# Kernel optimization log

Measured on AMD Instinct MI355X. Metric: run time of the kernel, lower is better.

## Reference

```python
import jax, jax.numpy as jnp
import numpy as np

N_HEADS = 16

def setup_inputs() -> dict:
    key = jax.random.key(0)
    k1, k2, k3, k4, k5 = jax.random.split(key, 5)
    B, S, D = 2, 2048, 1024
    x = jax.random.normal(k1, (B, S, D), dtype=jnp.float32)
    # parameters scaled ~ fan-in to keep softmax logits sane
    w_in = jax.random.normal(k2, (D, 3 * D), dtype=jnp.float32) * (1.0 / np.sqrt(D))
    b_in = jax.random.normal(k3, (3 * D,), dtype=jnp.float32) * 0.02
    w_out = jax.random.normal(k4, (D, D), dtype=jnp.float32) * (1.0 / np.sqrt(D))
    b_out = jax.random.normal(k5, (D,), dtype=jnp.float32) * 0.02
    return {"x": x, "w_in": w_in, "b_in": b_in, "w_out": w_out, "b_out": b_out,
            "causal_mask": 1}


def reference(x, w_in, b_in, w_out, b_out, causal_mask):
    B, S, D = x.shape
    H = N_HEADS
    dh = D // H
    qkv = x @ w_in + b_in                        # [B, S, 3D]
    q, k, v = jnp.split(qkv, 3, axis=-1)          # each [B, S, D]
    q = q.reshape(B, S, H, dh)
    k = k.reshape(B, S, H, dh)
    v = v.reshape(B, S, H, dh)
    # scores: [B, H, Sq, Sk]
    scores = jnp.einsum("bqhd,bkhd->bhqk", q, k)
    if causal_mask:
        mask = jnp.triu(jnp.ones((S, S), dtype=bool), k=1)
        scores = jnp.where(mask, -jnp.inf, scores)
    scores = scores / jnp.sqrt(jnp.asarray(dh, dtype=scores.dtype))
    weight = jax.nn.softmax(scores, axis=-1)
    out = jnp.einsum("bhqk,bkhd->bqhd", weight, v).reshape(B, S, D)
    return out @ w_out + b_out
```

## Files before the change

kernel.cpp:

```cpp
#include <hip/hip_runtime.h>
#include <hip/hip_bf16.h>

typedef __attribute__((ext_vector_type(8))) short short8;
typedef __attribute__((ext_vector_type(4))) short s16x4;
typedef __attribute__((ext_vector_type(4))) float f32x4;
typedef unsigned short u16;

__device__ inline u16 f2bf(float f) {
    union { float f; unsigned u; } x{f};
    unsigned r = (x.u + 0x7fff + ((x.u >> 16) & 1)) >> 16;
    return (u16)r;
}

__device__ inline unsigned pkbf(float hi, float lo) {
    unsigned a = __builtin_bit_cast(unsigned, hi) + 0x8000u;
    unsigned b = __builtin_bit_cast(unsigned, lo) + 0x8000u;
    return __builtin_amdgcn_perm(a, b, 0x07060302u);
}

__device__ inline void glds16(const u16* g, u16* l) {
    __builtin_amdgcn_global_load_lds(
        (const __attribute__((address_space(1))) void*)g,
        (__attribute__((address_space(3))) void*)l, 16, 0, 0);
}

__global__ __launch_bounds__(256) void prep(const float* __restrict__ x,
                                            const float* __restrict__ w_in,
                                            const float* __restrict__ w_out,
                                            u16* __restrict__ Xb,
                                            u16* __restrict__ WtIn,
                                            u16* __restrict__ WtOut) {
    __shared__ float tile[32][33];
    int bx = blockIdx.x, tid = threadIdx.x;
    if (bx < 4096) {
        int i = (bx * 256 + tid) * 4;
        float4 v = *(const float4*)&x[i];
        uint2 o;
        o.x = (unsigned)f2bf(v.x) | ((unsigned)f2bf(v.y) << 16);
        o.y = (unsigned)f2bf(v.z) | ((unsigned)f2bf(v.w) << 16);
        *(uint2*)&Xb[i] = o;
        return;
    }
    const float* W; u16* Wt; int K, N, n0, k0;
    if (bx < 7168) {
        int b2 = bx - 4096;
        W = w_in; Wt = WtIn; K = 1024; N = 3072;
        n0 = (b2 % 96) * 32; k0 = (b2 / 96) * 32;
    } else {
        int b3 = bx - 7168;
        W = w_out; Wt = WtOut; K = 1024; N = 1024;
        n0 = (b3 & 31) * 32; k0 = (b3 >> 5) * 32;
    }
    int tx = tid & 31, ty = tid >> 5;
    for (int i = 0; i < 32; i += 8)
        tile[ty + i][tx] = W[(size_t)(k0 + ty + i) * N + n0 + tx];
    __syncthreads();
    for (int i = 0; i < 32; i += 8)
        Wt[(size_t)(n0 + ty + i) * K + k0 + tx] = f2bf(tile[tx][ty + i]);
}

__global__ __launch_bounds__(256) void transpose_v(const u16* __restrict__ qkv,
                                                   u16* __restrict__ VT) {
    __shared__ u16 t[32][33];
    int s0 = blockIdx.x * 32, d0 = blockIdx.y * 32, bh = blockIdx.z;
    int b = bh >> 4, h = bh & 15;
    int tx = threadIdx.x, ty = threadIdx.y;
    const u16* Vp = qkv + (size_t)(b * 2048) * 3072 + 2048 + h * 64;
    for (int i = 0; i < 32; i += 8)
        t[ty + i][tx] = Vp[(size_t)(s0 + ty + i) * 3072 + d0 + tx];
    __syncthreads();
    u16* Vr = VT + (size_t)bh * 64 * 2048;
    for (int i = 0; i < 32; i += 8)
        Vr[(size_t)(d0 + ty + i) * 2048 + s0 + tx] = t[tx][ty + i];
}

#define BM 128
#define BN 128
#define BK 64
__global__ __launch_bounds__(256) void gemm_bt(const u16* __restrict__ A,
                                               const u16* __restrict__ Bt,
                                               const float* __restrict__ bias,
                                               void* __restrict__ C,
                                               int M, int N, int K, int c_is_f32,
                                               int qcols, float qscale) {
    __shared__ u16 smem[2 * BM * BK + 2048];
    u16* As = smem;
    u16* Bs = smem + BM * BK;

    int tid = threadIdx.x;
    int wave = tid >> 6, lane = tid & 63;
    int quad = lane >> 4, l16 = lane & 15;
    int wm = (wave >> 1) * 64, wn = (wave & 1) * 64;

    int nm = M / BM, nn = N / BN;
    const int GM = 8;
    int per_group = GM * nn;
    int group = blockIdx.x / per_group;
    int rem = blockIdx.x % per_group;
    int first_m = group * GM;
    int gsz = (nm - first_m < GM) ? (nm - first_m) : GM;
    int m0 = (first_m + rem % gsz) * BM;
    int n0 = (rem / gsz) * BN;

    f32x4 acc[4][4] = {};

    for (int k0 = 0; k0 < K; k0 += BK) {
        __syncthreads();
        for (int i = 0; i < 4; i++) {
            int c = tid + i * 256;
            int r = c >> 3, cc = c & 7;
            int gsrc = (cc ^ (r & 7)) * 8;
            glds16(&A[(size_t)(m0 + r) * K + k0 + gsrc], As + c * 8);
            glds16(&Bt[(size_t)(n0 + r) * K + k0 + gsrc], Bs + c * 8);
        }
        __syncthreads();
        for (int ks = 0; ks < 2; ks++) {
            short8 af[4], bf[4];
            for (int i = 0; i < 4; i++) {
                int row = wm + i * 16 + l16;
                int slot = (ks * 4 + quad) ^ (row & 7);
                af[i] = *(short8*)&As[row * BK + slot * 8];
            }
            for (int j = 0; j < 4; j++) {
                int row = wn + j * 16 + l16;
                int slot = (ks * 4 + quad) ^ (row & 7);
                bf[j] = *(short8*)&Bs[row * BK + slot * 8];
            }
            for (int i = 0; i < 4; i++)
                for (int j = 0; j < 4; j++)
                    acc[i][j] = __builtin_amdgcn_mfma_f32_16x16x32_bf16(
                        af[i], bf[j], acc[i][j], 0, 0, 0);
        }
    }

    if (c_is_f32) {
        for (int i = 0; i < 4; i++)
            for (int j = 0; j < 4; j++) {
                int col = n0 + wn + j * 16 + l16;
                float bv = bias ? bias[col] : 0.f;
                for (int r = 0; r < 4; r++) {
                    int row = m0 + wm + i * 16 + quad * 4 + r;
                    ((float*)C)[(size_t)row * N + col] = acc[i][j][r] + bv;
                }
            }
    } else {
        __syncthreads();
        u16 (*buf)[136] = (u16(*)[136])smem;
        for (int i = 0; i < 4; i++)
            for (int j = 0; j < 4; j++) {
                int col = wn + j * 16 + l16;
                float bv = bias ? bias[n0 + col] : 0.f;
                float scl = (n0 + col < qcols) ? qscale : 1.f;
                for (int r = 0; r < 4; r++)
                    buf[wm + i * 16 + quad * 4 + r][col] =
                        f2bf((acc[i][j][r] + bv) * scl);
            }
        __syncthreads();
        u16* Cb = (u16*)C;
        for (int it = 0; it < 8; it++) {
            int c = tid + it * 256;
            int row = c >> 4, k8 = c & 15;
            uint4 v = *(uint4*)&buf[row][k8 * 8];
            *(uint4*)&Cb[(size_t)(m0 + row) * N + n0 + k8 * 8] = v;
        }
    }
}

__global__ __launch_bounds__(512, 2) void attn_kernel(const u16* __restrict__ qkv,
                                                      const u16* __restrict__ VT,
                                                      u16* __restrict__ out) {
    const int S = 2048, D = 1024, stride = 3072;
    int idx = blockIdx.x;
    int p = idx >> 5, bh = idx & 31;
    int qtb[2] = {15 - p, p};
    int b = bh >> 4, h = bh & 15;
    int tid = threadIdx.x;
    int wave = tid >> 6, lane = tid & 63;
    int quad = lane >> 4, l16 = lane & 15;

    __shared__ u16 Klds[2][2][64 * 64];
    __shared__ u16 Vlds[2][2][64 * 64];
    __shared__ u16 Obuf[8][16][72];

    const u16* Qp = qkv + (size_t)(b * S) * stride + h * 64;
    const u16* Kp = Qp + D;
    const u16* Vtp = VT + (size_t)bh * 64 * S;

    short8 qf[2][2];
    for (int ph = 0; ph < 2; ph++) {
        int qrow = qtb[ph] * 128 + wave * 16 + l16;
        qf[ph][0] = *(const short8*)&Qp[(size_t)qrow * stride + quad * 8];
        qf[ph][1] = *(const short8*)&Qp[(size_t)qrow * stride + 32 + quad * 8];
    }

    int np0 = qtb[0] + 1;
    int ntp = np0 + qtb[1] + 1;

    auto stage = [&](int kt, int bsel, int ch) {
        int c = tid;
        int r = c >> 3, cc = c & 7;
        int gsrc = (cc ^ (r & 7)) * 8;
        glds16(&Kp[(size_t)(kt * 64 + r) * stride + gsrc], &Klds[bsel][ch][c * 8]);
        glds16(&Vtp[(size_t)r * S + kt * 64 + gsrc], &Vlds[bsel][ch][c * 8]);
    };

    stage(0, 0, 0);
    stage(1, 0, 1);

    f32x4 Oa[4] = {}, Ob[4] = {};
    float lsa = 0.f, lsb = 0.f;

    for (int jp = 0; jp < ntp; jp++) {
        int ph = (jp >= np0) ? 1 : 0;
        int j = ph ? jp - np0 : jp;
        int qt = qtb[ph];
        int ka = 2 * j, kb = 2 * j + 1;
        int cur = jp & 1;
        __syncthreads();
        if (jp + 1 < ntp) {
            int jp2 = jp + 1;
            int j2 = (jp2 >= np0) ? jp2 - np0 : jp2;
            stage(2 * j2, cur ^ 1, 0);
            stage(2 * j2 + 1, cur ^ 1, 1);
        }

        short8 kfa[4][2], kfb[4][2];
        for (int nb = 0; nb < 4; nb++) {
            int r = nb * 16 + l16;
            int s0 = ((0 + quad) ^ (r & 7)) * 8;
            int s1 = ((4 + quad) ^ (r & 7)) * 8;
            kfa[nb][0] = *(short8*)&Klds[cur][0][r * 64 + s0];
            kfa[nb][1] = *(short8*)&Klds[cur][0][r * 64 + s1];
            kfb[nb][0] = *(short8*)&Klds[cur][1][r * 64 + s0];
            kfb[nb][1] = *(short8*)&Klds[cur][1][r * 64 + s1];
        }
        f32x4 sta[4], stb[4];
        for (int nb = 0; nb < 4; nb++) {
            f32x4 t = {};
            t = __builtin_amdgcn_mfma_f32_16x16x32_bf16(kfa[nb][0], qf[ph][0], t, 0, 0, 0);
            t = __builtin_amdgcn_mfma_f32_16x16x32_bf16(kfa[nb][1], qf[ph][1], t, 0, 0, 0);
            sta[nb] = t;
            f32x4 u = {};
            u = __builtin_amdgcn_mfma_f32_16x16x32_bf16(kfb[nb][0], qf[ph][0], u, 0, 0, 0);
            u = __builtin_amdgcn_mfma_f32_16x16x32_bf16(kfb[nb][1], qf[ph][1], u, 0, 0, 0);
            stb[nb] = u;
        }

        if (j == qt) {
            int qabs = qt * 128 + wave * 16 + l16;
            for (int nb = 0; nb < 4; nb++) {
                int kba = ka * 64 + nb * 16 + quad * 4;
                int kbb = kb * 64 + nb * 16 + quad * 4;
                for (int r = 0; r < 4; r++) {
                    float ea = __builtin_amdgcn_exp2f(sta[nb][r]);
                    sta[nb][r] = (kba + r <= qabs) ? ea : 0.f;
                    float eb = __builtin_amdgcn_exp2f(stb[nb][r]);
                    stb[nb][r] = (kbb + r <= qabs) ? eb : 0.f;
                }
            }
        } else {
            for (int nb = 0; nb < 4; nb++)
                for (int r = 0; r < 4; r++) {
                    sta[nb][r] = __builtin_amdgcn_exp2f(sta[nb][r]);
                    stb[nb][r] = __builtin_amdgcn_exp2f(stb[nb][r]);
                }
        }

        s16x4 pfa[4], pfb[4];
        for (int nb = 0; nb < 4; nb++) {
            lsa += (sta[nb][0] + sta[nb][1]) + (sta[nb][2] + sta[nb][3]);
            lsb += (stb[nb][0] + stb[nb][1]) + (stb[nb][2] + stb[nb][3]);
            uint2 pk;
            pk.x = pkbf(sta[nb][1], sta[nb][0]);
            pk.y = pkbf(sta[nb][3], sta[nb][2]);
            pfa[nb] = __builtin_bit_cast(s16x4, pk);
            pk.x = pkbf(stb[nb][1], stb[nb][0]);
            pk.y = pkbf(stb[nb][3], stb[nb][2]);
            pfb[nb] = __builtin_bit_cast(s16x4, pk);
        }

        for (int db = 0; db < 4; db++) {
            int rr = db * 16 + l16;
            for (int kc = 0; kc < 4; kc++) {
                int g = kc * 2 + (quad >> 1);
                int slot = g ^ (rr & 7);
                int off = rr * 64 + slot * 8 + (quad & 1) * 4;
                s16x4 vfa = *(s16x4*)&Vlds[cur][0][off];
                Oa[db] = __builtin_amdgcn_mfma_f32_16x16x16bf16_1k(
                    pfa[kc], vfa, Oa[db], 0, 0, 0);
                s16x4 vfb = *(s16x4*)&Vlds[cur][1][off];
                Ob[db] = __builtin_amdgcn_mfma_f32_16x16x16bf16_1k(
                    pfb[kc], vfb, Ob[db], 0, 0, 0);
            }
        }

        if (jp == np0 - 1 || jp == ntp - 1) {
            float v = lsa + lsb;
            v += __shfl_xor(v, 16);
            v += __shfl_xor(v, 32);
            float rinv[4];
            for (int r = 0; r < 4; r++)
                rinv[r] = 1.f / __shfl(v, (lane & 48) | (quad * 4 + r));
            for (int db = 0; db < 4; db++)
                for (int r = 0; r < 4; r++)
                    Obuf[wave][quad * 4 + r][db * 16 + l16] =
                        f2bf((Oa[db][r] + Ob[db][r]) * rinv[r]);
            __asm__ volatile("s_waitcnt lgkmcnt(0)" ::: "memory");
            for (int i = 0; i < 2; i++) {
                int c = i * 64 + lane;
                int row = c >> 3, cc = c & 7;
                uint4 vv = *(uint4*)&Obuf[wave][row][cc * 8];
                int grow = qt * 128 + wave * 16 + row;
                *(uint4*)&out[(size_t)(b * S + grow) * D + h * 64 + cc * 8] = vv;
            }
            for (int db = 0; db < 4; db++) {
                Oa[db] = (f32x4){0.f, 0.f, 0.f, 0.f};
                Ob[db] = (f32x4){0.f, 0.f, 0.f, 0.f};
            }
            lsa = 0.f;
            lsb = 0.f;
        }
    }
}

extern "C" void kernel_launch(void* const* d_in, const int* in_sizes, int n_in,
                              void* d_out, int out_size, void* d_ws, size_t ws_size,
                              hipStream_t stream) {
    const float* x     = (const float*)d_in[0];
    const float* w_in  = (const float*)d_in[1];
    const float* b_in  = (const float*)d_in[2];
    const float* w_out = (const float*)d_in[3];
    const float* b_out = (const float*)d_in[4];

    const int Bsz = 2, S = 2048, D = 1024, H = 16;
    const int M = Bsz * S;
    const int N1 = 3 * D;
    const float sc = 0.125f * 1.44269504f;

    u16* ws    = (u16*)d_ws;
    u16* Xb    = ws;
    u16* WtIn  = Xb + (size_t)M * D;
    u16* WtOut = WtIn + (size_t)N1 * D;
    u16* qkvb  = WtOut + (size_t)D * D;
    u16* attnb = qkvb + (size_t)M * N1;
    u16* Vt    = Xb;

    prep<<<8192, 256, 0, stream>>>(x, w_in, w_out, Xb, WtIn, WtOut);
    gemm_bt<<<(M / BM) * (N1 / BN), 256, 0, stream>>>(Xb, WtIn, b_in, qkvb,
                                                      M, N1, D, 0, D, sc);
    transpose_v<<<dim3(S / 32, 2, Bsz * H), dim3(32, 8), 0, stream>>>(qkvb, Vt);
    attn_kernel<<<256, 512, 0, stream>>>(qkvb, Vt, attnb);
    gemm_bt<<<(M / BM) * (D / BN), 256, 0, stream>>>(attnb, WtOut, b_out, d_out,
                                                     M, D, D, 1, 0, 1.f);
}
```

Baseline: 185.3 us.

## Split attention blocks into one query tile each with 4 waves of 32 rows

The attention kernel previously ran 256 blocks of 512 threads, each handling a paired short and long causal query tile one after the other. It now launches 512 blocks of 256 threads, each handling a single query tile, with every wave covering 32 query rows so each K/V fragment loaded from LDS is reused across two row groups. The P·V MFMA operands are swapped so the output accumulator is transposed, which lets results be packed and stored straight to global memory without the LDS staging buffer. The trade-off is that the causal load balance from pairing tiles is lost, so per-block work is now uneven, and each lane holds more accumulator registers.

```diff
diff --git a/kernel.cpp b/kernel.cpp
--- a/kernel.cpp
+++ b/kernel.cpp
@@ -166,13 +166,15 @@
     }
 }
 
-__global__ __launch_bounds__(512, 2) void attn_kernel(const u16* __restrict__ qkv,
+__global__ __launch_bounds__(256, 2) void attn_kernel(const u16* __restrict__ qkv,
                                                       const u16* __restrict__ VT,
                                                       u16* __restrict__ out) {
     const int S = 2048, D = 1024, stride = 3072;
     int idx = blockIdx.x;
-    int p = idx >> 5, bh = idx & 31;
-    int qtb[2] = {15 - p, p};
+    int slot = idx >> 8;
+    int r5 = idx & 255;
+    int p = r5 >> 5, bh = r5 & 31;
+    int qt = slot ? p : 15 - p;
     int b = bh >> 4, h = bh & 15;
     int tid = threadIdx.x;
     int wave = tid >> 6, lane = tid & 63;
@@ -180,145 +182,120 @@
 
     __shared__ u16 Klds[2][2][64 * 64];
     __shared__ u16 Vlds[2][2][64 * 64];
-    __shared__ u16 Obuf[8][16][72];
 
     const u16* Qp = qkv + (size_t)(b * S) * stride + h * 64;
     const u16* Kp = Qp + D;
     const u16* Vtp = VT + (size_t)bh * 64 * S;
 
     short8 qf[2][2];
-    for (int ph = 0; ph < 2; ph++) {
-        int qrow = qtb[ph] * 128 + wave * 16 + l16;
-        qf[ph][0] = *(const short8*)&Qp[(size_t)qrow * stride + quad * 8];
-        qf[ph][1] = *(const short8*)&Qp[(size_t)qrow * stride + 32 + quad * 8];
-    }
-
-    int np0 = qtb[0] + 1;
-    int ntp = np0 + qtb[1] + 1;
+    for (int qh = 0; qh < 2; qh++) {
+        int qrow = qt * 128 + wave * 32 + qh * 16 + l16;
+        qf[qh][0] = *(const short8*)&Qp[(size_t)qrow * stride + quad * 8];
+        qf[qh][1] = *(const short8*)&Qp[(size_t)qrow * stride + 32 + quad * 8];
+    }
 
     auto stage = [&](int kt, int bsel, int ch) {
-        int c = tid;
-        int r = c >> 3, cc = c & 7;
-        int gsrc = (cc ^ (r & 7)) * 8;
-        glds16(&Kp[(size_t)(kt * 64 + r) * stride + gsrc], &Klds[bsel][ch][c * 8]);
-        glds16(&Vtp[(size_t)r * S + kt * 64 + gsrc], &Vlds[bsel][ch][c * 8]);
+        for (int i = 0; i < 2; i++) {
+            int c = tid + i * 256;
+            int rr = c >> 3, cc = c & 7;
+            int gsrc = (cc ^ (rr & 7)) * 8;
+            glds16(&Kp[(size_t)(kt * 64 + rr) * stride + gsrc],
+                   &Klds[bsel][ch][c * 8]);
+            glds16(&Vtp[(size_t)rr * S + kt * 64 + gsrc],
+                   &Vlds[bsel][ch][c * 8]);
+        }
     };
 
     stage(0, 0, 0);
     stage(1, 0, 1);
 
-    f32x4 Oa[4] = {}, Ob[4] = {};
-    float lsa = 0.f, lsb = 0.f;
-
-    for (int jp = 0; jp < ntp; jp++) {
-        int ph = (jp >= np0) ? 1 : 0;
-        int j = ph ? jp - np0 : jp;
-        int qt = qtb[ph];
-        int ka = 2 * j, kb = 2 * j + 1;
-        int cur = jp & 1;
-        __syncthreads();
-        if (jp + 1 < ntp) {
-            int jp2 = jp + 1;
-            int j2 = (jp2 >= np0) ? jp2 - np0 : jp2;
-            stage(2 * j2, cur ^ 1, 0);
-            stage(2 * j2 + 1, cur ^ 1, 1);
-        }
-
-        short8 kfa[4][2], kfb[4][2];
-        for (int nb = 0; nb < 4; nb++) {
-            int r = nb * 16 + l16;
-            int s0 = ((0 + quad) ^ (r & 7)) * 8;
-            int s1 = ((4 + quad) ^ (r & 7)) * 8;
-            kfa[nb][0] = *(short8*)&Klds[cur][0][r * 64 + s0];
-            kfa[nb][1] = *(short8*)&Klds[cur][0][r * 64 + s1];
-            kfb[nb][0] = *(short8*)&Klds[cur][1][r * 64 + s0];
-            kfb[nb][1] = *(short8*)&Klds[cur][1][r * 64 + s1];
-        }
-        f32x4 sta[4], stb[4];
-        for (int nb = 0; nb < 4; nb++) {
-            f32x4 t = {};
-            t = __builtin_amdgcn_mfma_f32_16x16x32_bf16(kfa[nb][0], qf[ph][0], t, 0, 0, 0);
-            t = __builtin_amdgcn_mfma_f32_16x16x32_bf16(kfa[nb][1], qf[ph][1], t, 0, 0, 0);
-            sta[nb] = t;
-            f32x4 u = {};
-            u = __builtin_amdgcn_mfma_f32_16x16x32_bf16(kfb[nb][0], qf[ph][0], u, 0, 0, 0);
-            u = __builtin_amdgcn_mfma_f32_16x16x32_bf16(kfb[nb][1], qf[ph][1], u, 0, 0, 0);
-            stb[nb] = u;
-        }
-
-        if (j == qt) {
-            int qabs = qt * 128 + wave * 16 + l16;
+    f32x4 O[4][2] = {};
+    float ls[2] = {0.f, 0.f};
+
+    int np = qt + 1;
+    for (int j = 0; j < np; j++) {
+        int cur = j & 1;
+        __syncthreads();
+        if (j + 1 < np) {
+            stage(2 * (j + 1), cur ^ 1, 0);
+            stage(2 * (j + 1) + 1, cur ^ 1, 1);
+        }
+        bool last = (j == qt);
+
+        s16x4 pf[2][2][4];
+        for (int ch = 0; ch < 2; ch++) {
+            short8 kf[4][2];
             for (int nb = 0; nb < 4; nb++) {
-                int kba = ka * 64 + nb * 16 + quad * 4;
-                int kbb = kb * 64 + nb * 16 + quad * 4;
-                for (int r = 0; r < 4; r++) {
-                    float ea = __builtin_amdgcn_exp2f(sta[nb][r]);
-                    sta[nb][r] = (kba + r <= qabs) ? ea : 0.f;
-                    float eb = __builtin_amdgcn_exp2f(stb[nb][r]);
-                    stb[nb][r] = (kbb + r <= qabs) ? eb : 0.f;
-                }
-            }
-        } else {
-            for (int nb = 0; nb < 4; nb++)
-                for (int r = 0; r < 4; r++) {
-                    sta[nb][r] = __builtin_amdgcn_exp2f(sta[nb][r]);
-                    stb[nb][r] = __builtin_amdgcn_exp2f(stb[nb][r]);
-                }
-        }
-
-        s16x4 pfa[4], pfb[4];
-        for (int nb = 0; nb < 4; nb++) {
-            lsa += (sta[nb][0] + sta[nb][1]) + (sta[nb][2] + sta[nb][3]);
-            lsb += (stb[nb][0] + stb[nb][1]) + (stb[nb][2] + stb[nb][3]);
-            uint2 pk;
-            pk.x = pkbf(sta[nb][1], sta[nb][0]);
-            pk.y = pkbf(sta[nb][3], sta[nb][2]);
-            pfa[nb] = __builtin_bit_cast(s16x4, pk);
-            pk.x = pkbf(stb[nb][1], stb[nb][0]);
-            pk.y = pkbf(stb[nb][3], stb[nb][2]);
-            pfb[nb] = __builtin_bit_cast(s16x4, pk);
+                int rr = nb * 16 + l16;
+                int s0 = ((0 + quad) ^ (rr & 7)) * 8;
+                int s1 = ((4 + quad) ^ (rr & 7)) * 8;
+                kf[nb][0] = *(short8*)&Klds[cur][ch][rr * 64 + s0];
+                kf[nb][1] = *(short8*)&Klds[cur][ch][rr * 64 + s1];
+            }
+            for (int qh = 0; qh < 2; qh++) {
+                f32x4 st[4];
+                for (int nb = 0; nb < 4; nb++) {
+                    f32x4 t = {};
+                    t = __builtin_amdgcn_mfma_f32_16x16x32_bf16(
+                        kf[nb][0], qf[qh][0], t, 0, 0, 0);
+                    t = __builtin_amdgcn_mfma_f32_16x16x32_bf16(
+                        kf[nb][1], qf[qh][1], t, 0, 0, 0);
+                    st[nb] = t;
+                }
+                if (last) {
+                    int qabs = qt * 128 + wave * 32 + qh * 16 + l16;
+                    for (int nb = 0; nb < 4; nb++) {
+                        int kb0 = (2 * j + ch) * 64 + nb * 16 + quad * 4;
+                        for (int r = 0; r < 4; r++) {
+                            float e = __builtin_amdgcn_exp2f(st[nb][r]);
+                            st[nb][r] = (kb0 + r <= qabs) ? e : 0.f;
+                        }
+                    }
+                } else {
+                    for (int nb = 0; nb < 4; nb++)
+                        for (int r = 0; r < 4; r++)
+                            st[nb][r] = __builtin_amdgcn_exp2f(st[nb][r]);
+                }
+                for (int nb = 0; nb < 4; nb++) {
+                    ls[qh] += (st[nb][0] + st[nb][1]) + (st[nb][2] + st[nb][3]);
+                    uint2 pk;
+                    pk.x = pkbf(st[nb][1], st[nb][0]);
+                    pk.y = pkbf(st[nb][3], st[nb][2]);
+                    pf[ch][qh][nb] = __builtin_bit_cast(s16x4, pk);
+                }
+            }
         }
 
         for (int db = 0; db < 4; db++) {
             int rr = db * 16 + l16;
             for (int kc = 0; kc < 4; kc++) {
                 int g = kc * 2 + (quad >> 1);
-                int slot = g ^ (rr & 7);
-                int off = rr * 64 + slot * 8 + (quad & 1) * 4;
+                int sl = g ^ (rr & 7);
+                int off = rr * 64 + sl * 8 + (quad & 1) * 4;
                 s16x4 vfa = *(s16x4*)&Vlds[cur][0][off];
-                Oa[db] = __builtin_amdgcn_mfma_f32_16x16x16bf16_1k(
-                    pfa[kc], vfa, Oa[db], 0, 0, 0);
                 s16x4 vfb = *(s16x4*)&Vlds[cur][1][off];
-                Ob[db] = __builtin_amdgcn_mfma_f32_16x16x16bf16_1k(
-                    pfb[kc], vfb, Ob[db], 0, 0, 0);
-            }
-        }
-
-        if (jp == np0 - 1 || jp == ntp - 1) {
-            float v = lsa + lsb;
-            v += __shfl_xor(v, 16);
-            v += __shfl_xor(v, 32);
-            float rinv[4];
-            for (int r = 0; r < 4; r++)
-                rinv[r] = 1.f / __shfl(v, (lane & 48) | (quad * 4 + r));
-            for (int db = 0; db < 4; db++)
-                for (int r = 0; r < 4; r++)
-                    Obuf[wave][quad * 4 + r][db * 16 + l16] =
-                        f2bf((Oa[db][r] + Ob[db][r]) * rinv[r]);
-            __asm__ volatile("s_waitcnt lgkmcnt(0)" ::: "memory");
-            for (int i = 0; i < 2; i++) {
-                int c = i * 64 + lane;
-                int row = c >> 3, cc = c & 7;
-                uint4 vv = *(uint4*)&Obuf[wave][row][cc * 8];
-                int grow = qt * 128 + wave * 16 + row;
-                *(uint4*)&out[(size_t)(b * S + grow) * D + h * 64 + cc * 8] = vv;
-            }
-            for (int db = 0; db < 4; db++) {
-                Oa[db] = (f32x4){0.f, 0.f, 0.f, 0.f};
-                Ob[db] = (f32x4){0.f, 0.f, 0.f, 0.f};
-            }
-            lsa = 0.f;
-            lsb = 0.f;
+                for (int qh = 0; qh < 2; qh++) {
+                    O[db][qh] = __builtin_amdgcn_mfma_f32_16x16x16bf16_1k(
+                        vfa, pf[0][qh][kc], O[db][qh], 0, 0, 0);
+                    O[db][qh] = __builtin_amdgcn_mfma_f32_16x16x16bf16_1k(
+                        vfb, pf[1][qh][kc], O[db][qh], 0, 0, 0);
+                }
+            }
+        }
+    }
+
+    for (int qh = 0; qh < 2; qh++) {
+        float v = ls[qh];
+        v += __shfl_xor(v, 16);
+        v += __shfl_xor(v, 32);
+        float rinv = 1.f / v;
+        int qrow = qt * 128 + wave * 32 + qh * 16 + l16;
+        for (int db = 0; db < 4; db++) {
+            uint2 o;
+            o.x = pkbf(O[db][qh][1] * rinv, O[db][qh][0] * rinv);
+            o.y = pkbf(O[db][qh][3] * rinv, O[db][qh][2] * rinv);
+            *(uint2*)&out[(size_t)(b * S + qrow) * D + h * 64 + db * 16 +
+                          quad * 4] = o;
         }
     }
 }
@@ -349,7 +326,7 @@
     gemm_bt<<<(M / BM) * (N1 / BN), 256, 0, stream>>>(Xb, WtIn, b_in, qkvb,
                                                       M, N1, D, 0, D, sc);
     transpose_v<<<dim3(S / 32, 2, Bsz * H), dim3(32, 8), 0, stream>>>(qkvb, Vt);
-    attn_kernel<<<256, 512, 0, stream>>>(qkvb, Vt, attnb);
+    attn_kernel<<<512, 256, 0, stream>>>(qkvb, Vt, attnb);
     gemm_bt<<<(M / BM) * (D / BN), 256, 0, stream>>>(attnb, WtOut, b_out, d_out,
                                                      M, D, D, 1, 0, 1.f);
 }
```

Result: no change. 184.3 us (-0.5%).
